# Optimization experiments

Hardware: AMD Instinct MI355X
Metric: run time of the kernel (lower is better)

The kernel has to match this reference:

```python
import jax, jax.numpy as jnp
import numpy as np

LAYER_SIZES = [256, 256, 256]
SPLIT_HALF = True
B, F0, D = 512, 32, 32


def setup_inputs() -> dict:
    key = jax.random.key(0)
    ks = jax.random.split(key, 7)
    field_nums = [F0]
    for i, s in enumerate(LAYER_SIZES):
        field_nums.append(s // 2 if (SPLIT_HALF and i != len(LAYER_SIZES) - 1) else (s // 2 if SPLIT_HALF else s))
    # field_nums = [32, 128, 128, 128] (last entry unused for weights)
    inp = {
        'feat': jax.random.normal(ks[0], (B, F0, D), dtype=jnp.float32),
        'W0': jax.random.normal(ks[1], (LAYER_SIZES[0], field_nums[0], F0), dtype=jnp.float32) * 0.05,
        'b0': jnp.zeros((LAYER_SIZES[0],), dtype=jnp.float32),
        'W1': jax.random.normal(ks[2], (LAYER_SIZES[1], field_nums[1], F0), dtype=jnp.float32) * 0.05,
        'b1': jnp.zeros((LAYER_SIZES[1],), dtype=jnp.float32),
        'W2': jax.random.normal(ks[3], (LAYER_SIZES[2], field_nums[2], F0), dtype=jnp.float32) * 0.05,
        'b2': jnp.zeros((LAYER_SIZES[2],), dtype=jnp.float32),
    }
    return inp


def _cin_layer(h, feat, W, b):
    # h: [B,H,D], feat: [B,F0,D], W: [K,H,F0], b: [K] -> out [B,K,D]
    # outer product per embedding dim, then 1x1 conv (full [H,F0] contraction)
    z = jnp.einsum('bid,bjd->bdij', h, feat)          # [B,D,H,F0]
    out = jnp.einsum('bdij,kij->bkd', z, W) + b[None, :, None]
    return jax.nn.relu(out)


def reference(feat, W0, b0, W1, b1, W2, b2):
    Ws = [W0, W1, W2]
    bs = [b0, b1, b2]
    h = feat
    p = []
    n_layers = len(LAYER_SIZES)
    for l, K in enumerate(LAYER_SIZES):
        out = _cin_layer(h, feat, Ws[l], bs[l])        # [B,K,D]
        if SPLIT_HALF and l != n_layers - 1:
            h = out[:, :K // 2, :]
            direct = out[:, K // 2:, :]
        else:
            direct = out
            h = out
        p.append(direct)
    return jnp.concatenate(p, axis=1).sum(-1)          # [B, sum of direct sizes]
```

## Files before the change

### kernel.cpp

```cpp
#include <hip/hip_runtime.h>
#include <hip/hip_fp16.h>
#include <stdint.h>


typedef _Float16 half8_t __attribute__((ext_vector_type(8)));
typedef float f32x4 __attribute__((ext_vector_type(4)));
typedef float f32x16 __attribute__((ext_vector_type(16)));
typedef uint32_t u32x4 __attribute__((ext_vector_type(4)));

union H8 {
  half8_t h;
  uint32_t u[4];
  u32x4 q;
};

#define AS1 __attribute__((address_space(1)))
#define AS3 __attribute__((address_space(3)))

static __device__ __forceinline__ uint32_t pkmul(uint32_t x, uint32_t y) {
  __half2 a = __builtin_bit_cast(__half2, x);
  __half2 b = __builtin_bit_cast(__half2, y);
  __half2 r = __hmul2(a, b);
  return __builtin_bit_cast(uint32_t, r);
}

static __device__ __forceinline__ uint32_t pack2h(float a, float b) {
  __half2 r = __floats2half2_rn(a, b);
  return __builtin_bit_cast(uint32_t, r);
}

__global__ void prep_kernel(const float* __restrict__ W0, const float* __restrict__ W1,
                            const float* __restrict__ W2, const float* __restrict__ feat,
                            uint16_t* __restrict__ Wt0, uint16_t* __restrict__ Wt1,
                            uint16_t* __restrict__ Wt2,
                            uint16_t* __restrict__ F16, uint32_t* __restrict__ hP0) {
  int blk = blockIdx.x;
  if (blk < 4608) {
    const float* W; uint16_t* Wt; int FLsh, base;
    if (blk < 512)       { W = W0; Wt = Wt0; FLsh = 5; base = 0; }
    else if (blk < 2560) { W = W1; Wt = Wt1; FLsh = 7; base = 512; }
    else                 { W = W2; Wt = Wt2; FLsh = 7; base = 2560; }
    int idx2 = (blk - base) * 256 + threadIdx.x;
    float2 xy = *(const float2*)(W + (size_t)idx2 * 2);
    int j2 = idx2 & 15;
    int i = (idx2 >> 4) & ((1 << FLsh) - 1);
    int k = idx2 >> (4 + FLsh);
    __half2 h2 = __floats2half2_rn(xy.x, xy.y);
    int g = j2 >> 2, kr = k & 15, kt = k >> 4;
    uint32_t* wt32 = (uint32_t*)Wt;
    wt32[(((size_t)i * 16 + kt) * 64 + g * 16 + kr) * 4 + (j2 & 3)] = *(uint32_t*)&h2;
  } else {
    int m = (blk - 4608) * 256 + threadIdx.x;
    int b = m >> 5, d = m & 31;
    const float* fb = feat + (size_t)b * 1024 + d;
    uint16_t hs[32];
#pragma unroll
    for (int j = 0; j < 32; ++j)
      hs[j] = __half_as_ushort(__float2half(fb[j * 32]));
    int mb = m >> 5, ml = m & 31;
#pragma unroll
    for (int jp = 0; jp < 16; ++jp) {
      uint32_t pr = (uint32_t)hs[2 * jp] | ((uint32_t)hs[2 * jp + 1] << 16);
      hP0[((size_t)(mb * 4 + (jp >> 2)) * 32 + ml) * 4 + (jp & 3)] = pr;
    }
#pragma unroll
    for (int c = 0; c < 4; ++c) {
      u32x4 q;
      q[0] = (uint32_t)hs[c * 8 + 0] | ((uint32_t)hs[c * 8 + 1] << 16);
      q[1] = (uint32_t)hs[c * 8 + 2] | ((uint32_t)hs[c * 8 + 3] << 16);
      q[2] = (uint32_t)hs[c * 8 + 4] | ((uint32_t)hs[c * 8 + 5] << 16);
      q[3] = (uint32_t)hs[c * 8 + 6] | ((uint32_t)hs[c * 8 + 7] << 16);
      *(u32x4*)(F16 + (size_t)m * 32 + c * 8) = q;
    }
  }
}

template <int FL>
__global__ __launch_bounds__(1024, 4) void gemm_cin(
    const uint32_t* __restrict__ hP,
    const uint16_t* __restrict__ wt,
    const uint16_t* __restrict__ f16m,
    const float* __restrict__ bias,
    uint32_t* __restrict__ houtP,
    float* __restrict__ outp,
    int obase, int klo) {
  __shared__ __align__(16) char smem[131072];
  const int tid = threadIdx.x;
  const int lane = tid & 63, w = tid >> 6;
  const int l31 = lane & 31, l5 = lane >> 5;
  const int bx = blockIdx.x;
  const int kg = bx & 7, mg = bx >> 3;
  const int mb = mg * 16 + w;

  const uint16_t* fbase = f16m + (size_t)(mb * 32 + l31) * 32 + l5 * 8;
  H8 ff0, ff1;
  ff0.q = *(const u32x4*)(fbase);
  ff1.q = *(const u32x4*)(fbase + 16);

  const uint32_t* hbase = hP + (size_t)mb * (FL / 8) * 128 + l31 * 4;
  u32x4 hqA[4], hqB[4];

  const char* wsrc = (const char*)wt + kg * 2048;

#define CIN_STAGE(QN, BUFOFS)                                                     \
  _Pragma("unroll") for (int c_ = 0; c_ < 4; ++c_) {                              \
    int u_ = w * 4 + c_;                                                          \
    __builtin_amdgcn_global_load_lds(                                             \
        (const AS1 uint32_t*)(wsrc + (size_t)((QN) * 32 + (u_ >> 1)) * 16384 +    \
                              (u_ & 1) * 1024 + lane * 16),                       \
        (AS3 uint32_t*)(smem + (BUFOFS) + u_ * 1024 + lane * 16), 16, 0, 0);      \
  }

#define CIN_HLOAD(QN, HQ)                                                         \
  _Pragma("unroll") for (int c_ = 0; c_ < 4; ++c_)                                \
      HQ[c_] = *(const u32x4*)(hbase + ((QN) * 4 + c_) * 128);

  CIN_STAGE(0, 0)
  CIN_HLOAD(0, hqA)

  f32x16 acc = {};

  const char* rb = smem + ((l31 >> 4) << 10) + (l5 << 8) + ((lane & 15) << 4);

  __syncthreads();

#define CIN_Q(HQ, RBOFS)                                                          \
  {                                                                               \
    const char* rb_ = rb + (RBOFS);                                               \
    _Pragma("unroll") for (int s = 0; s < 32; ++s) {                              \
      uint32_t hp_ = HQ[s >> 3][(s >> 1) & 3];                                    \
      uint32_t e_ =                                                               \
          __builtin_amdgcn_perm(hp_, hp_, (s & 1) ? 0x03020302u : 0x01000100u);   \
      H8 wf0_, wf1_, b0_, b1_;                                                    \
      wf0_.q = *(const u32x4*)(rb_ + s * 2048);                                   \
      wf1_.q = *(const u32x4*)(rb_ + s * 2048 + 512);                             \
      _Pragma("unroll") for (int c_ = 0; c_ < 4; ++c_) {                          \
        b0_.u[c_] = pkmul(ff0.u[c_], e_);                                         \
        b1_.u[c_] = pkmul(ff1.u[c_], e_);                                         \
      }                                                                           \
      __builtin_amdgcn_s_setprio(1);                                              \
      acc = __builtin_amdgcn_mfma_f32_32x32x16_f16(wf0_.h, b0_.h, acc, 0, 0, 0);  \
      acc = __builtin_amdgcn_mfma_f32_32x32x16_f16(wf1_.h, b1_.h, acc, 0, 0, 0);  \
      __builtin_amdgcn_s_setprio(0);                                              \
    }                                                                             \
  }

  if (FL == 32) {
    CIN_Q(hqA, 0)
  } else {
    CIN_STAGE(1, 65536)
    CIN_HLOAD(1, hqB)
    CIN_Q(hqA, 0)
    __syncthreads();
    CIN_STAGE(2, 0)
    CIN_HLOAD(2, hqA)
    CIN_Q(hqB, 65536)
    __syncthreads();
    CIN_STAGE(3, 65536)
    CIN_HLOAD(3, hqB)
    CIN_Q(hqA, 0)
    __syncthreads();
    CIN_Q(hqB, 65536)
  }
#undef CIN_Q
#undef CIN_STAGE
#undef CIN_HLOAD

  f32x4 bv[4];
#pragma unroll
  for (int a = 0; a < 4; ++a)
    bv[a] = *(const f32x4*)(bias + kg * 32 + a * 8 + l5 * 4);
  float v[16];
#pragma unroll
  for (int a = 0; a < 4; ++a)
#pragma unroll
    for (int t = 0; t < 4; ++t) {
      float x = acc[a * 4 + t] + bv[a][t];
      v[a * 4 + t] = x > 0.f ? x : 0.f;
    }

  if (houtP != nullptr && kg < 4) {
#pragma unroll
    for (int a = 0; a < 4; ++a)
#pragma unroll
      for (int c = 0; c < 2; ++c) {
        uint32_t pr = pack2h(v[a * 4 + 2 * c], v[a * 4 + 2 * c + 1]);
        houtP[((size_t)(mb * 16 + kg * 4 + a) * 32 + l31) * 4 + 2 * l5 + c] = pr;
      }
  }

#pragma unroll
  for (int r = 0; r < 16; ++r) {
    float x = v[r];
    x += __shfl_xor(x, 1);
    x += __shfl_xor(x, 2);
    x += __shfl_xor(x, 4);
    x += __shfl_xor(x, 8);
    x += __shfl_xor(x, 16);
    v[r] = x;
  }
  if (kg * 32 >= klo && (lane == 0 || lane == 32)) {
    float* ob = outp + (size_t)mb * 512 + obase + kg * 32 - klo + l5 * 4;
#pragma unroll
    for (int a = 0; a < 4; ++a)
      *(f32x4*)(ob + a * 8) = (f32x4){v[a * 4], v[a * 4 + 1], v[a * 4 + 2], v[a * 4 + 3]};
  }
}

extern "C" void kernel_launch(void* const* d_in, const int* in_sizes, int n_in,
                              void* d_out, int out_size, void* d_ws, size_t ws_size,
                              hipStream_t stream) {
  const float* feat = (const float*)d_in[0];
  const float* W0 = (const float*)d_in[1];
  const float* b0 = (const float*)d_in[2];
  const float* W1 = (const float*)d_in[3];
  const float* b1 = (const float*)d_in[4];
  const float* W2 = (const float*)d_in[5];
  const float* b2 = (const float*)d_in[6];
  float* out = (float*)d_out;
  char* ws = (char*)d_ws;

  uint16_t* Wt0 = (uint16_t*)(ws + 0x000000);
  uint16_t* Wt1 = (uint16_t*)(ws + 0x080000);
  uint16_t* Wt2 = (uint16_t*)(ws + 0x280000);
  uint16_t* F16 = (uint16_t*)(ws + 0x480000);
  uint32_t* hP0 = (uint32_t*)(ws + 0x580000);
  uint32_t* hP1 = (uint32_t*)(ws + 0x680000);
  uint32_t* hP2 = (uint32_t*)(ws + 0xA80000);

  prep_kernel<<<4672, 256, 0, stream>>>(W0, W1, W2, feat, Wt0, Wt1, Wt2, F16, hP0);

  gemm_cin<32><<<256, 1024, 0, stream>>>(hP0, Wt0, F16, b0, hP1, out, 0, 128);
  gemm_cin<128><<<256, 1024, 0, stream>>>(hP1, Wt1, F16, b1, hP2, out, 128, 128);
  gemm_cin<128><<<256, 1024, 0, stream>>>(hP2, Wt2, F16, b2, (uint32_t*)nullptr,
                                          out, 256, 0);
}
```

Baseline: 106.2 us.

## Restructure CIN GEMM: 256-thread blocks, two batch rows per wave, finer double buffering

Blocks shrink from 1024 to 256 threads. Each wave now computes two batch rows (mb0 and mb0+1) that share each LDS weight fragment load, which halves LDS weight reads per MFMA. Weights are staged in 16-slice chunks with a 2x32KB double buffer and raw waitcnt/barrier, and the grid doubles to 512 blocks. The h-packing layout changes to lane-contiguous scalar loads, and the prep and epilogue writers are updated to match. The cost is more accumulator registers and a less flexible occupancy bound.

```diff
diff --git a/kernel.cpp b/kernel.cpp
--- a/kernel.cpp
+++ b/kernel.cpp
@@ -61,7 +61,7 @@
 #pragma unroll
     for (int jp = 0; jp < 16; ++jp) {
       uint32_t pr = (uint32_t)hs[2 * jp] | ((uint32_t)hs[2 * jp + 1] << 16);
-      hP0[((size_t)(mb * 4 + (jp >> 2)) * 32 + ml) * 4 + (jp & 3)] = pr;
+      hP0[((size_t)(mb * 4 + (jp >> 2)) * 4 + (jp & 3)) * 32 + ml] = pr;
     }
 #pragma unroll
     for (int c = 0; c < 4; ++c) {
@@ -76,7 +76,7 @@
 }
 
 template <int FL>
-__global__ __launch_bounds__(1024, 4) void gemm_cin(
+__global__ __launch_bounds__(256) void gemm_cin(
     const uint32_t* __restrict__ hP,
     const uint16_t* __restrict__ wt,
     const uint16_t* __restrict__ f16m,
@@ -84,127 +84,147 @@
     uint32_t* __restrict__ houtP,
     float* __restrict__ outp,
     int obase, int klo) {
-  __shared__ __align__(16) char smem[131072];
+  constexpr int NCH = FL / 16;
+  __shared__ __align__(16) char smem[65536];
   const int tid = threadIdx.x;
   const int lane = tid & 63, w = tid >> 6;
   const int l31 = lane & 31, l5 = lane >> 5;
-  const int bx = blockIdx.x;
-  const int kg = bx & 7, mg = bx >> 3;
-  const int mb = mg * 16 + w;
-
-  const uint16_t* fbase = f16m + (size_t)(mb * 32 + l31) * 32 + l5 * 8;
-  H8 ff0, ff1;
-  ff0.q = *(const u32x4*)(fbase);
-  ff1.q = *(const u32x4*)(fbase + 16);
-
-  const uint32_t* hbase = hP + (size_t)mb * (FL / 8) * 128 + l31 * 4;
-  u32x4 hqA[4], hqB[4];
-
-  const char* wsrc = (const char*)wt + kg * 2048;
-
-#define CIN_STAGE(QN, BUFOFS)                                                     \
-  _Pragma("unroll") for (int c_ = 0; c_ < 4; ++c_) {                              \
-    int u_ = w * 4 + c_;                                                          \
-    __builtin_amdgcn_global_load_lds(                                             \
-        (const AS1 uint32_t*)(wsrc + (size_t)((QN) * 32 + (u_ >> 1)) * 16384 +    \
-                              (u_ & 1) * 1024 + lane * 16),                       \
-        (AS3 uint32_t*)(smem + (BUFOFS) + u_ * 1024 + lane * 16), 16, 0, 0);      \
-  }
-
-#define CIN_HLOAD(QN, HQ)                                                         \
-  _Pragma("unroll") for (int c_ = 0; c_ < 4; ++c_)                                \
-      HQ[c_] = *(const u32x4*)(hbase + ((QN) * 4 + c_) * 128);
-
-  CIN_STAGE(0, 0)
-  CIN_HLOAD(0, hqA)
-
-  f32x16 acc = {};
-
+  const int kg = blockIdx.x & 7, mgrp = blockIdx.x >> 3;
+  const int mb0 = mgrp * 8 + w * 2;
+
+  const char* wsrc = (const char*)wt + kg * 2048 + (size_t)(tid >> 7) * 16384 +
+                     (tid & 127) * 16;
+  char* sdst = smem + tid * 16;
+
+#define STAGE(Q)                                                              \
+  { _Pragma("unroll") for (int c_ = 0; c_ < 8; ++c_)                          \
+      __builtin_amdgcn_global_load_lds(                                       \
+          (const AS1 uint32_t*)(wsrc + (size_t)((Q) * 16 + c_ * 2) * 16384),  \
+          (AS3 uint32_t*)(sdst + ((Q) & 1) * 32768 + c_ * 4096), 16, 0, 0); }
+
+  const uint32_t* hbA = hP + (size_t)mb0 * (FL / 8) * 128 + l31;
+  const uint32_t* hbB = hbA + (size_t)(FL / 8) * 128;
+
+#define HLD(HB, Q, G, DST)                                                    \
+  { const uint32_t* p_ = (HB) + ((Q) * 2 + (G)) * 128;                        \
+    DST[0] = p_[0]; DST[1] = p_[32]; DST[2] = p_[64]; DST[3] = p_[96]; }
+
+  STAGE(0)
+  if (NCH > 1) STAGE(1)
+  u32x4 hA0, hA1, hB0, hB1, nA0, nA1, nB0, nB1;
+  HLD(hbA, 0, 0, hA0) HLD(hbA, 0, 1, hA1)
+  HLD(hbB, 0, 0, hB0) HLD(hbB, 0, 1, hB1)
+
+  const uint16_t* fb0 = f16m + (size_t)(mb0 * 32 + l31) * 32 + l5 * 8;
+  H8 ffA0, ffA1, ffB0, ffB1;
+  ffA0.q = *(const u32x4*)(fb0);
+  ffA1.q = *(const u32x4*)(fb0 + 16);
+  ffB0.q = *(const u32x4*)(fb0 + 1024);
+  ffB1.q = *(const u32x4*)(fb0 + 1040);
+
+  f32x16 accA = {}, accB = {};
   const char* rb = smem + ((l31 >> 4) << 10) + (l5 << 8) + ((lane & 15) << 4);
 
-  __syncthreads();
-
-#define CIN_Q(HQ, RBOFS)                                                          \
-  {                                                                               \
-    const char* rb_ = rb + (RBOFS);                                               \
-    _Pragma("unroll") for (int s = 0; s < 32; ++s) {                              \
-      uint32_t hp_ = HQ[s >> 3][(s >> 1) & 3];                                    \
-      uint32_t e_ =                                                               \
-          __builtin_amdgcn_perm(hp_, hp_, (s & 1) ? 0x03020302u : 0x01000100u);   \
-      H8 wf0_, wf1_, b0_, b1_;                                                    \
-      wf0_.q = *(const u32x4*)(rb_ + s * 2048);                                   \
-      wf1_.q = *(const u32x4*)(rb_ + s * 2048 + 512);                             \
-      _Pragma("unroll") for (int c_ = 0; c_ < 4; ++c_) {                          \
-        b0_.u[c_] = pkmul(ff0.u[c_], e_);                                         \
-        b1_.u[c_] = pkmul(ff1.u[c_], e_);                                         \
-      }                                                                           \
-      __builtin_amdgcn_s_setprio(1);                                              \
-      acc = __builtin_amdgcn_mfma_f32_32x32x16_f16(wf0_.h, b0_.h, acc, 0, 0, 0);  \
-      acc = __builtin_amdgcn_mfma_f32_32x32x16_f16(wf1_.h, b1_.h, acc, 0, 0, 0);  \
-      __builtin_amdgcn_s_setprio(0);                                              \
-    }                                                                             \
-  }
-
-  if (FL == 32) {
-    CIN_Q(hqA, 0)
-  } else {
-    CIN_STAGE(1, 65536)
-    CIN_HLOAD(1, hqB)
-    CIN_Q(hqA, 0)
-    __syncthreads();
-    CIN_STAGE(2, 0)
-    CIN_HLOAD(2, hqA)
-    CIN_Q(hqB, 65536)
-    __syncthreads();
-    CIN_STAGE(3, 65536)
-    CIN_HLOAD(3, hqB)
-    CIN_Q(hqA, 0)
-    __syncthreads();
-    CIN_Q(hqB, 65536)
-  }
-#undef CIN_Q
-#undef CIN_STAGE
-#undef CIN_HLOAD
+  asm volatile("s_waitcnt vmcnt(0)" ::: "memory");
+  asm volatile("s_barrier" ::: "memory");
+
+#define CSTEP(S, HCA, HCB, RBQ)                                                    \
+  {                                                                                \
+    uint32_t hA_ = HCA[((S) >> 1) & 3], hB_ = HCB[((S) >> 1) & 3];                 \
+    uint32_t sel_ = ((S) & 1) ? 0x03020302u : 0x01000100u;                         \
+    uint32_t eA_ = __builtin_amdgcn_perm(hA_, hA_, sel_);                          \
+    uint32_t eB_ = __builtin_amdgcn_perm(hB_, hB_, sel_);                          \
+    H8 wf0_, wf1_, bA0_, bA1_, bB0_, bB1_;                                         \
+    wf0_.q = *(const u32x4*)((RBQ) + (S) * 2048);                                  \
+    wf1_.q = *(const u32x4*)((RBQ) + (S) * 2048 + 512);                            \
+    _Pragma("unroll") for (int c_ = 0; c_ < 4; ++c_) {                             \
+      bA0_.u[c_] = pkmul(ffA0.u[c_], eA_);                                         \
+      bA1_.u[c_] = pkmul(ffA1.u[c_], eA_);                                         \
+      bB0_.u[c_] = pkmul(ffB0.u[c_], eB_);                                         \
+      bB1_.u[c_] = pkmul(ffB1.u[c_], eB_);                                         \
+    }                                                                              \
+    accA = __builtin_amdgcn_mfma_f32_32x32x16_f16(wf0_.h, bA0_.h, accA, 0, 0, 0);  \
+    accA = __builtin_amdgcn_mfma_f32_32x32x16_f16(wf1_.h, bA1_.h, accA, 0, 0, 0);  \
+    accB = __builtin_amdgcn_mfma_f32_32x32x16_f16(wf0_.h, bB0_.h, accB, 0, 0, 0);  \
+    accB = __builtin_amdgcn_mfma_f32_32x32x16_f16(wf1_.h, bB1_.h, accB, 0, 0, 0);  \
+  }
+
+#define CHUNK(Q, CA0, CA1, CB0, CB1, NA0_, NA1_, NB0_, NB1_)                  \
+  {                                                                           \
+    const char* rbq_ = rb + ((Q) & 1) * 32768;                                \
+    CSTEP(0, CA0, CB0, rbq_) CSTEP(1, CA0, CB0, rbq_)                         \
+    if ((Q) + 1 < NCH) {                                                      \
+      HLD(hbA, (Q) + 1, 0, NA0_) HLD(hbA, (Q) + 1, 1, NA1_)                   \
+      HLD(hbB, (Q) + 1, 0, NB0_) HLD(hbB, (Q) + 1, 1, NB1_)                   \
+    }                                                                         \
+    CSTEP(2, CA0, CB0, rbq_) CSTEP(3, CA0, CB0, rbq_)                         \
+    CSTEP(4, CA0, CB0, rbq_) CSTEP(5, CA0, CB0, rbq_)                         \
+    CSTEP(6, CA0, CB0, rbq_) CSTEP(7, CA0, CB0, rbq_)                         \
+    CSTEP(8, CA1, CB1, rbq_) CSTEP(9, CA1, CB1, rbq_)                         \
+    CSTEP(10, CA1, CB1, rbq_) CSTEP(11, CA1, CB1, rbq_)                       \
+    CSTEP(12, CA1, CB1, rbq_) CSTEP(13, CA1, CB1, rbq_)                       \
+    CSTEP(14, CA1, CB1, rbq_) CSTEP(15, CA1, CB1, rbq_)                       \
+  }
+
+#define BOUNDARY(QS)                                                          \
+  {                                                                           \
+    asm volatile("s_waitcnt vmcnt(0)" ::: "memory");                          \
+    asm volatile("s_barrier" ::: "memory");                                   \
+    if ((QS) < NCH) STAGE(QS)                                                 \
+  }
+
+#pragma unroll 1
+  for (int qq = 0; qq < NCH; qq += 2) {
+    CHUNK(qq, hA0, hA1, hB0, hB1, nA0, nA1, nB0, nB1)
+    BOUNDARY(qq + 2)
+    CHUNK(qq + 1, nA0, nA1, nB0, nB1, hA0, hA1, hB0, hB1)
+    if (qq + 2 < NCH) BOUNDARY(qq + 3)
+  }
+#undef CHUNK
+#undef CSTEP
+#undef BOUNDARY
+#undef STAGE
+#undef HLD
 
   f32x4 bv[4];
 #pragma unroll
   for (int a = 0; a < 4; ++a)
     bv[a] = *(const f32x4*)(bias + kg * 32 + a * 8 + l5 * 4);
-  float v[16];
-#pragma unroll
-  for (int a = 0; a < 4; ++a)
-#pragma unroll
-    for (int t = 0; t < 4; ++t) {
-      float x = acc[a * 4 + t] + bv[a][t];
-      v[a * 4 + t] = x > 0.f ? x : 0.f;
-    }
-
-  if (houtP != nullptr && kg < 4) {
-#pragma unroll
-    for (int a = 0; a < 4; ++a)
-#pragma unroll
-      for (int c = 0; c < 2; ++c) {
-        uint32_t pr = pack2h(v[a * 4 + 2 * c], v[a * 4 + 2 * c + 1]);
-        houtP[((size_t)(mb * 16 + kg * 4 + a) * 32 + l31) * 4 + 2 * l5 + c] = pr;
-      }
-  }
-
-#pragma unroll
-  for (int r = 0; r < 16; ++r) {
-    float x = v[r];
-    x += __shfl_xor(x, 1);
-    x += __shfl_xor(x, 2);
-    x += __shfl_xor(x, 4);
-    x += __shfl_xor(x, 8);
-    x += __shfl_xor(x, 16);
-    v[r] = x;
-  }
-  if (kg * 32 >= klo && (lane == 0 || lane == 32)) {
-    float* ob = outp + (size_t)mb * 512 + obase + kg * 32 - klo + l5 * 4;
-#pragma unroll
-    for (int a = 0; a < 4; ++a)
-      *(f32x4*)(ob + a * 8) = (f32x4){v[a * 4], v[a * 4 + 1], v[a * 4 + 2], v[a * 4 + 3]};
-  }
+
+#define EPILOG(ACC, MB)                                                           \
+  {                                                                               \
+    float v[16];                                                                  \
+    _Pragma("unroll") for (int a = 0; a < 4; ++a)                                 \
+        _Pragma("unroll") for (int t = 0; t < 4; ++t) {                           \
+      float x = ACC[a * 4 + t] + bv[a][t];                                        \
+      v[a * 4 + t] = x > 0.f ? x : 0.f;                                           \
+    }                                                                             \
+    if (houtP != nullptr && kg < 4) {                                             \
+      _Pragma("unroll") for (int a = 0; a < 4; ++a)                               \
+          _Pragma("unroll") for (int c = 0; c < 2; ++c) {                         \
+        uint32_t pr = pack2h(v[a * 4 + 2 * c], v[a * 4 + 2 * c + 1]);             \
+        houtP[((size_t)((MB) * 16 + kg * 4 + a) * 4 + 2 * l5 + c) * 32 + l31] =   \
+            pr;                                                                   \
+      }                                                                           \
+    }                                                                             \
+    _Pragma("unroll") for (int r = 0; r < 16; ++r) {                              \
+      float x = v[r];                                                             \
+      x += __shfl_xor(x, 1); x += __shfl_xor(x, 2);                               \
+      x += __shfl_xor(x, 4); x += __shfl_xor(x, 8);                               \
+      x += __shfl_xor(x, 16);                                                     \
+      v[r] = x;                                                                   \
+    }                                                                             \
+    if (kg * 32 >= klo && (lane == 0 || lane == 32)) {                            \
+      float* ob = outp + (size_t)(MB) * 512 + obase + kg * 32 - klo + l5 * 4;     \
+      _Pragma("unroll") for (int a = 0; a < 4; ++a)                               \
+          *(f32x4*)(ob + a * 8) =                                                 \
+              (f32x4){v[a * 4], v[a * 4 + 1], v[a * 4 + 2], v[a * 4 + 3]};        \
+    }                                                                             \
+  }
+
+  EPILOG(accA, mb0)
+  EPILOG(accB, mb0 + 1)
+#undef EPILOG
 }
 
 extern "C" void kernel_launch(void* const* d_in, const int* in_sizes, int n_in,
@@ -230,8 +250,8 @@
 
   prep_kernel<<<4672, 256, 0, stream>>>(W0, W1, W2, feat, Wt0, Wt1, Wt2, F16, hP0);
 
-  gemm_cin<32><<<256, 1024, 0, stream>>>(hP0, Wt0, F16, b0, hP1, out, 0, 128);
-  gemm_cin<128><<<256, 1024, 0, stream>>>(hP1, Wt1, F16, b1, hP2, out, 128, 128);
-  gemm_cin<128><<<256, 1024, 0, stream>>>(hP2, Wt2, F16, b2, (uint32_t*)nullptr,
-                                          out, 256, 0);
-}
+  gemm_cin<32><<<512, 256, 0, stream>>>(hP0, Wt0, F16, b0, hP1, out, 0, 128);
+  gemm_cin<128><<<512, 256, 0, stream>>>(hP1, Wt1, F16, b1, hP2, out, 128, 128);
+  gemm_cin<128><<<512, 256, 0, stream>>>(hP2, Wt2, F16, b2, (uint32_t*)nullptr,
+                                         out, 256, 0);
+}
```

Result: faster. 95.34 us (-10.2%).

## Fuse three CIN layers into one persistent kernel keeping hidden state in LDS

Applied to the files above, without the earlier changes.

Replaces the three per-layer GEMM launches with a single kernel in which each block owns two batch rows for all layers. The hidden state stays in LDS between layers, and weights stream through a double-buffered LDS ring that prefetches across layer boundaries. The weight prep kernel is also vectorized to 16-byte loads and stores. This removes two launches and the global round trips for the hidden state, but each block now streams every weight chunk. Parallelism also drops to 256 blocks of 8 waves, each holding four accumulators.

```diff
diff --git a/kernel.cpp b/kernel.cpp
--- a/kernel.cpp
+++ b/kernel.cpp
@@ -33,35 +33,40 @@
                             const float* __restrict__ W2, const float* __restrict__ feat,
                             uint16_t* __restrict__ Wt0, uint16_t* __restrict__ Wt1,
                             uint16_t* __restrict__ Wt2,
-                            uint16_t* __restrict__ F16, uint32_t* __restrict__ hP0) {
+                            uint16_t* __restrict__ F16, uint32_t* __restrict__ hL0) {
   int blk = blockIdx.x;
-  if (blk < 4608) {
+  if (blk < 1152) {
     const float* W; uint16_t* Wt; int FLsh, base;
-    if (blk < 512)       { W = W0; Wt = Wt0; FLsh = 5; base = 0; }
-    else if (blk < 2560) { W = W1; Wt = Wt1; FLsh = 7; base = 512; }
-    else                 { W = W2; Wt = Wt2; FLsh = 7; base = 2560; }
-    int idx2 = (blk - base) * 256 + threadIdx.x;
-    float2 xy = *(const float2*)(W + (size_t)idx2 * 2);
-    int j2 = idx2 & 15;
-    int i = (idx2 >> 4) & ((1 << FLsh) - 1);
-    int k = idx2 >> (4 + FLsh);
-    __half2 h2 = __floats2half2_rn(xy.x, xy.y);
-    int g = j2 >> 2, kr = k & 15, kt = k >> 4;
-    uint32_t* wt32 = (uint32_t*)Wt;
-    wt32[(((size_t)i * 16 + kt) * 64 + g * 16 + kr) * 4 + (j2 & 3)] = *(uint32_t*)&h2;
+    if (blk < 128)      { W = W0; Wt = Wt0; FLsh = 5; base = 0; }
+    else if (blk < 640) { W = W1; Wt = Wt1; FLsh = 7; base = 128; }
+    else                { W = W2; Wt = Wt2; FLsh = 7; base = 640; }
+    int idx4 = (blk - base) * 256 + threadIdx.x;
+    int jg = idx4 & 3;
+    int i = (idx4 >> 2) & ((1 << FLsh) - 1);
+    int k = idx4 >> (2 + FLsh);
+    const float* src = W + ((size_t)(k << FLsh) + i) * 32 + jg * 8;
+    float4 x0 = *(const float4*)(src);
+    float4 x1 = *(const float4*)(src + 4);
+    u32x4 o;
+    o[0] = pack2h(x0.x, x0.y);
+    o[1] = pack2h(x0.z, x0.w);
+    o[2] = pack2h(x1.x, x1.y);
+    o[3] = pack2h(x1.z, x1.w);
+    int kr = k & 15, kt = k >> 4;
+    *(u32x4*)((uint32_t*)Wt + (((size_t)i * 16 + kt) * 64 + jg * 16 + kr) * 4) = o;
   } else {
-    int m = (blk - 4608) * 256 + threadIdx.x;
+    int m = (blk - 1152) * 256 + threadIdx.x;
     int b = m >> 5, d = m & 31;
     const float* fb = feat + (size_t)b * 1024 + d;
     uint16_t hs[32];
 #pragma unroll
     for (int j = 0; j < 32; ++j)
       hs[j] = __half_as_ushort(__float2half(fb[j * 32]));
-    int mb = m >> 5, ml = m & 31;
-#pragma unroll
-    for (int jp = 0; jp < 16; ++jp) {
-      uint32_t pr = (uint32_t)hs[2 * jp] | ((uint32_t)hs[2 * jp + 1] << 16);
-      hP0[((size_t)(mb * 4 + (jp >> 2)) * 32 + ml) * 4 + (jp & 3)] = pr;
+    int mt = m >> 6, mbh = (m >> 5) & 1, ml = m & 31;
+#pragma unroll
+    for (int i2 = 0; i2 < 16; ++i2) {
+      uint32_t pr = (uint32_t)hs[2 * i2] | ((uint32_t)hs[2 * i2 + 1] << 16);
+      hL0[(size_t)mt * 1024 + i2 * 64 + ml * 2 + mbh] = pr;
     }
 #pragma unroll
     for (int c = 0; c < 4; ++c) {
@@ -75,136 +80,161 @@
   }
 }
 
-template <int FL>
-__global__ __launch_bounds__(1024, 4) void gemm_cin(
-    const uint32_t* __restrict__ hP,
-    const uint16_t* __restrict__ wt,
+template <int NCHK, bool PRODH>
+__device__ __forceinline__ void cin_layer(
+    const char* wlay, const char* wnext, const float* __restrict__ bias,
+    float* __restrict__ outp, int obase, int klo,
+    char* hlds, char* ring0, char* ring1,
+    int tid, int w, int l31, int l5, int lane, int mt,
+    const H8& ffA0, const H8& ffA1, const H8& ffB0, const H8& ffB1) {
+  f32x16 accA0 = {}, accA1 = {}, accB0 = {}, accB1 = {};
+  char* rcur = ring0;
+  char* rnxt = ring1;
+  const int rboff = w * 2048 + ((l31 >> 4) << 10) + (l5 << 8) + ((l31 & 15) << 4);
+
+#pragma unroll 1
+  for (int q = 0; q < NCHK; ++q) {
+    asm volatile("s_waitcnt vmcnt(0)" ::: "memory");
+    __builtin_amdgcn_s_barrier();
+    const char* src = (q + 1 < NCHK) ? wlay + (size_t)(q + 1) * 65536 : wnext;
+#pragma unroll
+    for (int c = 0; c < 8; ++c)
+      __builtin_amdgcn_global_load_lds(
+          (const AS1 uint32_t*)(src + c * 8192 + tid * 16),
+          (AS3 uint32_t*)(rnxt + c * 8192 + tid * 16), 16, 0, 0);
+    uint2 hu0 = *(const uint2*)(hlds + q * 512 + l31 * 8);
+    uint2 hu1 = *(const uint2*)(hlds + q * 512 + 256 + l31 * 8);
+    const char* rb = rcur + rboff;
+#pragma unroll
+    for (int s = 0; s < 4; ++s) {
+      H8 wf0, wf1;
+      wf0.q = *(const u32x4*)(rb + s * 16384);
+      wf1.q = *(const u32x4*)(rb + s * 16384 + 512);
+      uint32_t hx = (s < 2) ? hu0.x : hu1.x;
+      uint32_t hy = (s < 2) ? hu0.y : hu1.y;
+      uint32_t psel = (s & 1) ? 0x03020302u : 0x01000100u;
+      uint32_t eA = __builtin_amdgcn_perm(hx, hx, psel);
+      uint32_t eB = __builtin_amdgcn_perm(hy, hy, psel);
+      H8 bA0, bA1, bB0, bB1;
+#pragma unroll
+      for (int c = 0; c < 4; ++c) {
+        bA0.u[c] = pkmul(ffA0.u[c], eA);
+        bA1.u[c] = pkmul(ffA1.u[c], eA);
+        bB0.u[c] = pkmul(ffB0.u[c], eB);
+        bB1.u[c] = pkmul(ffB1.u[c], eB);
+      }
+      accA0 = __builtin_amdgcn_mfma_f32_32x32x16_f16(wf0.h, bA0.h, accA0, 0, 0, 0);
+      accB0 = __builtin_amdgcn_mfma_f32_32x32x16_f16(wf0.h, bB0.h, accB0, 0, 0, 0);
+      accA1 = __builtin_amdgcn_mfma_f32_32x32x16_f16(wf1.h, bA1.h, accA1, 0, 0, 0);
+      accB1 = __builtin_amdgcn_mfma_f32_32x32x16_f16(wf1.h, bB1.h, accB1, 0, 0, 0);
+    }
+    char* t = rcur; rcur = rnxt; rnxt = t;
+  }
+
+  f32x16 accA = accA0 + accA1;
+  f32x16 accB = accB0 + accB1;
+  f32x4 bv[4];
+#pragma unroll
+  for (int a = 0; a < 4; ++a)
+    bv[a] = *(const f32x4*)(bias + w * 32 + a * 8 + l5 * 4);
+  float vA[16], vB[16];
+#pragma unroll
+  for (int a = 0; a < 4; ++a)
+#pragma unroll
+    for (int t = 0; t < 4; ++t) {
+      float x = accA[a * 4 + t] + bv[a][t];
+      vA[a * 4 + t] = x > 0.f ? x : 0.f;
+      float y = accB[a * 4 + t] + bv[a][t];
+      vB[a * 4 + t] = y > 0.f ? y : 0.f;
+    }
+
+  if (PRODH) {
+    __syncthreads();
+    if (w < 4) {
+#pragma unroll
+      for (int a = 0; a < 4; ++a)
+#pragma unroll
+        for (int c = 0; c < 2; ++c) {
+          int i2 = w * 16 + 4 * a + 2 * l5 + c;
+          uint2 pr;
+          pr.x = pack2h(vA[a * 4 + 2 * c], vA[a * 4 + 2 * c + 1]);
+          pr.y = pack2h(vB[a * 4 + 2 * c], vB[a * 4 + 2 * c + 1]);
+          *(uint2*)(hlds + i2 * 256 + l31 * 8) = pr;
+        }
+    }
+  }
+
+#pragma unroll
+  for (int r = 0; r < 16; ++r) {
+    float x = vA[r];
+    x += __shfl_xor(x, 1); x += __shfl_xor(x, 2);
+    x += __shfl_xor(x, 4); x += __shfl_xor(x, 8);
+    x += __shfl_xor(x, 16);
+    vA[r] = x;
+    float y = vB[r];
+    y += __shfl_xor(y, 1); y += __shfl_xor(y, 2);
+    y += __shfl_xor(y, 4); y += __shfl_xor(y, 8);
+    y += __shfl_xor(y, 16);
+    vB[r] = y;
+  }
+  if (w * 32 >= klo && (lane == 0 || lane == 32)) {
+    float* obA = outp + (size_t)(mt * 2) * 512 + obase + w * 32 - klo + l5 * 4;
+#pragma unroll
+    for (int a = 0; a < 4; ++a) {
+      *(f32x4*)(obA + a * 8) =
+          (f32x4){vA[a * 4], vA[a * 4 + 1], vA[a * 4 + 2], vA[a * 4 + 3]};
+      *(f32x4*)(obA + 512 + a * 8) =
+          (f32x4){vB[a * 4], vB[a * 4 + 1], vB[a * 4 + 2], vB[a * 4 + 3]};
+    }
+  }
+  if (PRODH) __syncthreads();
+}
+
+__global__ __launch_bounds__(512, 2) void cin_fused(
+    const uint32_t* __restrict__ hL0g,
+    const uint16_t* __restrict__ wt0, const uint16_t* __restrict__ wt1,
+    const uint16_t* __restrict__ wt2,
     const uint16_t* __restrict__ f16m,
-    const float* __restrict__ bias,
-    uint32_t* __restrict__ houtP,
-    float* __restrict__ outp,
-    int obase, int klo) {
-  __shared__ __align__(16) char smem[131072];
+    const float* __restrict__ b0, const float* __restrict__ b1,
+    const float* __restrict__ b2,
+    float* __restrict__ outp) {
+  __shared__ __align__(16) char smem[147456];
+  char* hlds = smem;
+  char* ring0 = smem + 16384;
+  char* ring1 = smem + 81920;
   const int tid = threadIdx.x;
   const int lane = tid & 63, w = tid >> 6;
   const int l31 = lane & 31, l5 = lane >> 5;
-  const int bx = blockIdx.x;
-  const int kg = bx & 7, mg = bx >> 3;
-  const int mb = mg * 16 + w;
-
-  const uint16_t* fbase = f16m + (size_t)(mb * 32 + l31) * 32 + l5 * 8;
-  H8 ff0, ff1;
-  ff0.q = *(const u32x4*)(fbase);
-  ff1.q = *(const u32x4*)(fbase + 16);
-
-  const uint32_t* hbase = hP + (size_t)mb * (FL / 8) * 128 + l31 * 4;
-  u32x4 hqA[4], hqB[4];
-
-  const char* wsrc = (const char*)wt + kg * 2048;
-
-#define CIN_STAGE(QN, BUFOFS)                                                     \
-  _Pragma("unroll") for (int c_ = 0; c_ < 4; ++c_) {                              \
-    int u_ = w * 4 + c_;                                                          \
-    __builtin_amdgcn_global_load_lds(                                             \
-        (const AS1 uint32_t*)(wsrc + (size_t)((QN) * 32 + (u_ >> 1)) * 16384 +    \
-                              (u_ & 1) * 1024 + lane * 16),                       \
-        (AS3 uint32_t*)(smem + (BUFOFS) + u_ * 1024 + lane * 16), 16, 0, 0);      \
-  }
-
-#define CIN_HLOAD(QN, HQ)                                                         \
-  _Pragma("unroll") for (int c_ = 0; c_ < 4; ++c_)                                \
-      HQ[c_] = *(const u32x4*)(hbase + ((QN) * 4 + c_) * 128);
-
-  CIN_STAGE(0, 0)
-  CIN_HLOAD(0, hqA)
-
-  f32x16 acc = {};
-
-  const char* rb = smem + ((l31 >> 4) << 10) + (l5 << 8) + ((lane & 15) << 4);
-
-  __syncthreads();
-
-#define CIN_Q(HQ, RBOFS)                                                          \
-  {                                                                               \
-    const char* rb_ = rb + (RBOFS);                                               \
-    _Pragma("unroll") for (int s = 0; s < 32; ++s) {                              \
-      uint32_t hp_ = HQ[s >> 3][(s >> 1) & 3];                                    \
-      uint32_t e_ =                                                               \
-          __builtin_amdgcn_perm(hp_, hp_, (s & 1) ? 0x03020302u : 0x01000100u);   \
-      H8 wf0_, wf1_, b0_, b1_;                                                    \
-      wf0_.q = *(const u32x4*)(rb_ + s * 2048);                                   \
-      wf1_.q = *(const u32x4*)(rb_ + s * 2048 + 512);                             \
-      _Pragma("unroll") for (int c_ = 0; c_ < 4; ++c_) {                          \
-        b0_.u[c_] = pkmul(ff0.u[c_], e_);                                         \
-        b1_.u[c_] = pkmul(ff1.u[c_], e_);                                         \
-      }                                                                           \
-      __builtin_amdgcn_s_setprio(1);                                              \
-      acc = __builtin_amdgcn_mfma_f32_32x32x16_f16(wf0_.h, b0_.h, acc, 0, 0, 0);  \
-      acc = __builtin_amdgcn_mfma_f32_32x32x16_f16(wf1_.h, b1_.h, acc, 0, 0, 0);  \
-      __builtin_amdgcn_s_setprio(0);                                              \
-    }                                                                             \
-  }
-
-  if (FL == 32) {
-    CIN_Q(hqA, 0)
-  } else {
-    CIN_STAGE(1, 65536)
-    CIN_HLOAD(1, hqB)
-    CIN_Q(hqA, 0)
-    __syncthreads();
-    CIN_STAGE(2, 0)
-    CIN_HLOAD(2, hqA)
-    CIN_Q(hqB, 65536)
-    __syncthreads();
-    CIN_STAGE(3, 65536)
-    CIN_HLOAD(3, hqB)
-    CIN_Q(hqA, 0)
-    __syncthreads();
-    CIN_Q(hqB, 65536)
-  }
-#undef CIN_Q
-#undef CIN_STAGE
-#undef CIN_HLOAD
-
-  f32x4 bv[4];
-#pragma unroll
-  for (int a = 0; a < 4; ++a)
-    bv[a] = *(const f32x4*)(bias + kg * 32 + a * 8 + l5 * 4);
-  float v[16];
-#pragma unroll
-  for (int a = 0; a < 4; ++a)
-#pragma unroll
-    for (int t = 0; t < 4; ++t) {
-      float x = acc[a * 4 + t] + bv[a][t];
-      v[a * 4 + t] = x > 0.f ? x : 0.f;
-    }
-
-  if (houtP != nullptr && kg < 4) {
-#pragma unroll
-    for (int a = 0; a < 4; ++a)
-#pragma unroll
-      for (int c = 0; c < 2; ++c) {
-        uint32_t pr = pack2h(v[a * 4 + 2 * c], v[a * 4 + 2 * c + 1]);
-        houtP[((size_t)(mb * 16 + kg * 4 + a) * 32 + l31) * 4 + 2 * l5 + c] = pr;
-      }
-  }
-
-#pragma unroll
-  for (int r = 0; r < 16; ++r) {
-    float x = v[r];
-    x += __shfl_xor(x, 1);
-    x += __shfl_xor(x, 2);
-    x += __shfl_xor(x, 4);
-    x += __shfl_xor(x, 8);
-    x += __shfl_xor(x, 16);
-    v[r] = x;
-  }
-  if (kg * 32 >= klo && (lane == 0 || lane == 32)) {
-    float* ob = outp + (size_t)mb * 512 + obase + kg * 32 - klo + l5 * 4;
-#pragma unroll
-    for (int a = 0; a < 4; ++a)
-      *(f32x4*)(ob + a * 8) = (f32x4){v[a * 4], v[a * 4 + 1], v[a * 4 + 2], v[a * 4 + 3]};
-  }
+  const int mt = blockIdx.x;
+
+  if (tid < 256)
+    __builtin_amdgcn_global_load_lds(
+        (const AS1 uint32_t*)(hL0g + (size_t)mt * 1024 + tid * 4),
+        (AS3 uint32_t*)(hlds + tid * 16), 16, 0, 0);
+  const char* w0b = (const char*)wt0;
+  const char* w1b = (const char*)wt1;
+  const char* w2b = (const char*)wt2;
+#pragma unroll
+  for (int c = 0; c < 8; ++c)
+    __builtin_amdgcn_global_load_lds(
+        (const AS1 uint32_t*)(w0b + c * 8192 + tid * 16),
+        (AS3 uint32_t*)(ring0 + c * 8192 + tid * 16), 16, 0, 0);
+
+  const uint16_t* fb0 = f16m + ((size_t)mt * 64 + l31) * 32 + l5 * 8;
+  H8 ffA0, ffA1, ffB0, ffB1;
+  ffA0.q = *(const u32x4*)(fb0);
+  ffA1.q = *(const u32x4*)(fb0 + 16);
+  ffB0.q = *(const u32x4*)(fb0 + 1024);
+  ffB1.q = *(const u32x4*)(fb0 + 1040);
+
+  cin_layer<8, true>(w0b, w1b, b0, outp, 0, 128, hlds, ring0, ring1,
+                     tid, w, l31, l5, lane, mt, ffA0, ffA1, ffB0, ffB1);
+  cin_layer<32, true>(w1b, w2b, b1, outp, 128, 128, hlds, ring0, ring1,
+                      tid, w, l31, l5, lane, mt, ffA0, ffA1, ffB0, ffB1);
+  cin_layer<32, false>(w2b, w2b, b2, outp, 256, 0, hlds, ring0, ring1,
+                       tid, w, l31, l5, lane, mt, ffA0, ffA1, ffB0, ffB1);
+
+  asm volatile("s_waitcnt vmcnt(0)" ::: "memory");
 }
 
 extern "C" void kernel_launch(void* const* d_in, const int* in_sizes, int n_in,
@@ -224,14 +254,9 @@
   uint16_t* Wt1 = (uint16_t*)(ws + 0x080000);
   uint16_t* Wt2 = (uint16_t*)(ws + 0x280000);
   uint16_t* F16 = (uint16_t*)(ws + 0x480000);
-  uint32_t* hP0 = (uint32_t*)(ws + 0x580000);
-  uint32_t* hP1 = (uint32_t*)(ws + 0x680000);
-  uint32_t* hP2 = (uint32_t*)(ws + 0xA80000);
-
-  prep_kernel<<<4672, 256, 0, stream>>>(W0, W1, W2, feat, Wt0, Wt1, Wt2, F16, hP0);
-
-  gemm_cin<32><<<256, 1024, 0, stream>>>(hP0, Wt0, F16, b0, hP1, out, 0, 128);
-  gemm_cin<128><<<256, 1024, 0, stream>>>(hP1, Wt1, F16, b1, hP2, out, 128, 128);
-  gemm_cin<128><<<256, 1024, 0, stream>>>(hP2, Wt2, F16, b2, (uint32_t*)nullptr,
-                                          out, 256, 0);
-}
+  uint32_t* hL0 = (uint32_t*)(ws + 0x580000);
+
+  prep_kernel<<<1216, 256, 0, stream>>>(W0, W1, W2, feat, Wt0, Wt1, Wt2, F16, hL0);
+
+  cin_fused<<<256, 512, 0, stream>>>(hL0, Wt0, Wt1, Wt2, F16, b0, b1, b2, out);
+}
```

After: 104.5 us. About the same (-1.6%).
